# Kernel optimization log

Measured on AMD Instinct MI355X. Metric: run time of the kernel, lower is better.

The kernel has to match this reference:

```python
import jax, jax.numpy as jnp
import numpy as np

BITS = 8
BOUND = 2 ** (BITS - 1) - 1  # 127, symmetric int8 as in AQT IntNumerics


def setup_inputs() -> dict:
    key = jax.random.key(0)
    k1, k2 = jax.random.split(key)
    lhs = jax.random.normal(k1, (8192, 4096), dtype=jnp.float32)
    rhs = jax.random.normal(k2, (4096, 4096), dtype=jnp.float32)
    return {"lhs": lhs, "rhs": rhs}


def reference(lhs, rhs):
    # Per-channel symmetric scales over the contracting dim (AQT calibration:
    # abs-max / bound). lhs contracts axis 1, rhs contracts axis 0, per
    # dimension_numbers (((1,),(0,)),((),())).
    lhs_scale = jnp.max(jnp.abs(lhs), axis=1, keepdims=True) / BOUND  # [M,1]
    rhs_scale = jnp.max(jnp.abs(rhs), axis=0, keepdims=True) / BOUND  # [1,N]
    lhs_scale = jnp.where(lhs_scale == 0, jnp.ones_like(lhs_scale), lhs_scale)
    rhs_scale = jnp.where(rhs_scale == 0, jnp.ones_like(rhs_scale), rhs_scale)

    # Quantize: round-to-nearest, clip to [-127, 127], store as int8.
    qlhs = jnp.clip(jnp.round(lhs / lhs_scale), -BOUND, BOUND).astype(jnp.int8)
    qrhs = jnp.clip(jnp.round(rhs / rhs_scale), -BOUND, BOUND).astype(jnp.int8)

    # Integer matmul with int32 accumulation (the AQT quantized dot_general).
    acc = jax.lax.dot_general(
        qlhs, qrhs,
        dimension_numbers=(((1,), (0,)), ((), ())),
        preferred_element_type=jnp.int32,
    )  # [M, N] int32

    # Inline dequant by transposed scales (scale_t): [M,1] * [1,N].
    return acc.astype(jnp.float32) * lhs_scale * rhs_scale
```

## Files before the change

### kernel.cpp

```cpp
#include <hip/hip_runtime.h>
#include <stdint.h>

#define M_DIM 8192
#define N_DIM 4096
#define K_DIM 4096

typedef int v4i __attribute__((ext_vector_type(4)));

typedef __attribute__((address_space(1))) const void gas_void;
typedef __attribute__((address_space(3))) void las_void;

__device__ __forceinline__ void async_copy16(const uint8_t* g, uint8_t* l) {
    __builtin_amdgcn_global_load_lds((gas_void*)g, (las_void*)l, 16, 0, 0);
}

__device__ __forceinline__ int quant1(float x, float scale) {
    float q = __builtin_rintf(x / scale);
    q = fminf(127.0f, fmaxf(-127.0f, q));
    return (int)q;
}

__device__ __forceinline__ uint32_t pack4(int q0, int q1, int q2, int q3) {
    return (uint32_t)(q0 & 255) | ((uint32_t)(q1 & 255) << 8) |
           ((uint32_t)(q2 & 255) << 16) | ((uint32_t)(q3 & 255) << 24);
}

__global__ __launch_bounds__(256) void quant_lhs_kernel(
    const float* __restrict__ lhs, uint8_t* __restrict__ qlhs,
    float* __restrict__ lhs_scale) {
    const int row = blockIdx.x;
    const int tid = threadIdx.x;
    const float4* src = (const float4*)(lhs + (size_t)row * K_DIM);

    float4 v[4];
    float m = 0.0f;
#pragma unroll
    for (int i = 0; i < 4; ++i) {
        v[i] = src[tid + i * 256];
        m = fmaxf(m, fmaxf(fmaxf(fabsf(v[i].x), fabsf(v[i].y)),
                           fmaxf(fabsf(v[i].z), fabsf(v[i].w))));
    }
#pragma unroll
    for (int off = 32; off > 0; off >>= 1)
        m = fmaxf(m, __shfl_down(m, off, 64));

    __shared__ float wmax[4];
    if ((tid & 63) == 0) wmax[tid >> 6] = m;
    __syncthreads();
    const float mm = fmaxf(fmaxf(wmax[0], wmax[1]), fmaxf(wmax[2], wmax[3]));
    const float scale = (mm == 0.0f) ? 1.0f : mm / 127.0f;
    if (tid == 0) lhs_scale[row] = scale;

    uint32_t* dst = (uint32_t*)(qlhs + (size_t)row * K_DIM);
#pragma unroll
    for (int i = 0; i < 4; ++i) {
        dst[tid + i * 256] = pack4(quant1(v[i].x, scale), quant1(v[i].y, scale),
                                   quant1(v[i].z, scale), quant1(v[i].w, scale));
    }
}

__global__ __launch_bounds__(256) void rhs_max_kernel(
    const float* __restrict__ rhs, uint32_t* __restrict__ maxbits) {
    const int c = blockIdx.x * 256 + threadIdx.x;
    const int r0 = blockIdx.y * 32;
    float m = 0.0f;
#pragma unroll
    for (int r = 0; r < 32; ++r)
        m = fmaxf(m, fabsf(rhs[(size_t)(r0 + r) * N_DIM + c]));
    atomicMax(&maxbits[c], __float_as_uint(m));
}

__global__ __launch_bounds__(256) void quant_rhs_t_kernel(
    const float* __restrict__ rhs, const uint32_t* __restrict__ maxbits,
    uint8_t* __restrict__ qrhsT) {
    __shared__ __align__(16) uint8_t tile[64 * 132];
    const int nbase = blockIdx.x * 64;
    const int kbase = blockIdx.y * 128;
    const int tid = threadIdx.x;

    const int n0 = (tid & 15) * 4;
    float s[4];
#pragma unroll
    for (int j = 0; j < 4; ++j) {
        const float m = __uint_as_float(maxbits[nbase + n0 + j]);
        s[j] = (m == 0.0f) ? 1.0f : m / 127.0f;
    }

#pragma unroll
    for (int p = 0; p < 2; ++p) {
        const int k0 = (tid >> 4) * 4 + p * 64;
        int q[4][4];
#pragma unroll
        for (int i = 0; i < 4; ++i) {
            const float4 v = *(const float4*)(
                rhs + (size_t)(kbase + k0 + i) * N_DIM + nbase + n0);
            q[i][0] = quant1(v.x, s[0]);
            q[i][1] = quant1(v.y, s[1]);
            q[i][2] = quant1(v.z, s[2]);
            q[i][3] = quant1(v.w, s[3]);
        }
#pragma unroll
        for (int j = 0; j < 4; ++j) {
            *(uint32_t*)(tile + (n0 + j) * 132 + k0) =
                pack4(q[0][j], q[1][j], q[2][j], q[3][j]);
        }
    }
    __syncthreads();

#pragma unroll
    for (int p = 0; p < 2; ++p) {
        const int c = tid + p * 256;
        const int n = c >> 3;
        const int g = c & 7;
        uint32_t d[4];
#pragma unroll
        for (int w = 0; w < 4; ++w)
            d[w] = *(const uint32_t*)(tile + n * 132 + g * 16 + w * 4);
        uint4 u;
        u.x = d[0]; u.y = d[1]; u.z = d[2]; u.w = d[3];
        *(uint4*)(qrhsT + (size_t)(nbase + n) * K_DIM + kbase + g * 16) = u;
    }
}

__global__ __launch_bounds__(512, 2) void gemm_i8_kernel(
    const uint8_t* __restrict__ qlhs, const uint8_t* __restrict__ qrhsT,
    const float* __restrict__ lhs_scale, const uint32_t* __restrict__ maxbits,
    float* __restrict__ out) {
    extern __shared__ __align__(16) uint8_t smem[];

    const int tid = threadIdx.x;
    const int wave = tid >> 6;
    const int lane = tid & 63;

    const int bm = blockIdx.y * 256;
    const int bn = blockIdx.x * 256;

    const int srow = tid >> 2;
    const int gsrc = (((tid & 3) ^ ((tid >> 3) & 3)) << 4);
    const uint8_t* gA = qlhs + (size_t)(bm + srow) * K_DIM + gsrc;
    const uint8_t* gA2 = gA + (size_t)128 * K_DIM;
    const uint8_t* gB = qrhsT + (size_t)(bn + srow) * K_DIM + gsrc;
    const uint8_t* gB2 = gB + (size_t)128 * K_DIM;
    const uint32_t stO = (uint32_t)tid * 16u;

    const int wm = (wave >> 2) * 128;
    const int wn = (wave & 3) * 64;
    const uint32_t fg = (uint32_t)((((lane >> 4) ^ ((lane >> 1) & 3)) << 4));
    const uint32_t aoff = (uint32_t)((wm + (lane & 15)) * 64) + fg;
    const uint32_t boff = 16384u + (uint32_t)((wn + (lane & 15)) * 64) + fg;

    v4i acc[8][4] = {};

#define BARRIER() __builtin_amdgcn_s_barrier()
#define LGKM0()                                            \
    do {                                                   \
        asm volatile("s_waitcnt lgkmcnt(0)" ::: "memory"); \
        __builtin_amdgcn_sched_barrier(0);                 \
    } while (0)

#pragma unroll
    for (int p = 0; p < 3; ++p) {
        uint8_t* sb = smem + (p << 15);
        async_copy16(gA, sb + stO);
        async_copy16(gA2, sb + 8192 + stO);
        async_copy16(gB, sb + 16384 + stO);
        async_copy16(gB2, sb + 24576 + stO);
        gA += 64; gA2 += 64; gB += 64; gB2 += 64;
    }
    asm volatile("s_waitcnt vmcnt(8)" ::: "memory");
    BARRIER();

#pragma unroll 1
    for (int tt = 0; tt < 64; tt += 4) {
#pragma unroll
        for (int u = 0; u < 4; ++u) {
            const int t = tt + u;
            uint8_t* const Cb = smem + (u << 15);
            uint8_t* const Sb = smem + (((u + 3) & 3) << 15);

            v4i a[4], b[4];

#pragma unroll
            for (int i = 0; i < 4; ++i)
                a[i] = *(const v4i*)(Cb + aoff + i * 1024);
#pragma unroll
            for (int i = 0; i < 4; ++i)
                b[i] = *(const v4i*)(Cb + boff + i * 1024);
            async_copy16(gA, Sb + stO);
            async_copy16(gA2, Sb + 8192 + stO);
            BARRIER();
            LGKM0();
            __builtin_amdgcn_s_setprio(1);
#pragma unroll
            for (int mi = 0; mi < 4; ++mi)
#pragma unroll
                for (int ni = 0; ni < 4; ++ni)
                    acc[mi][ni] = __builtin_amdgcn_mfma_i32_16x16x64_i8(
                        a[mi], b[ni], acc[mi][ni], 0, 0, 0);
            __builtin_amdgcn_s_setprio(0);
            BARRIER();

#pragma unroll
            for (int i = 0; i < 4; ++i)
                a[i] = *(const v4i*)(Cb + aoff + (4 + i) * 1024);
            async_copy16(gB, Sb + 16384 + stO);
            async_copy16(gB2, Sb + 24576 + stO);
            if (t < 60) {
                gA += 64; gA2 += 64; gB += 64; gB2 += 64;
            }
            BARRIER();
            LGKM0();
            __builtin_amdgcn_s_setprio(1);
#pragma unroll
            for (int mi = 0; mi < 4; ++mi)
#pragma unroll
                for (int ni = 0; ni < 4; ++ni)
                    acc[4 + mi][ni] = __builtin_amdgcn_mfma_i32_16x16x64_i8(
                        a[mi], b[ni], acc[4 + mi][ni], 0, 0, 0);
            __builtin_amdgcn_s_setprio(0);
            asm volatile("s_waitcnt vmcnt(8)" ::: "memory");
            BARRIER();
        }
    }
    asm volatile("s_waitcnt vmcnt(0)" ::: "memory");

    const int r0 = bm + wm + (lane >> 4) * 4;
    const int c0 = bn + wn + (lane & 15);
    float rsv[4];
#pragma unroll
    for (int ni = 0; ni < 4; ++ni) {
        const float m = __uint_as_float(maxbits[c0 + ni * 16]);
        rsv[ni] = (m == 0.0f) ? 1.0f : m / 127.0f;
    }
#pragma unroll
    for (int mi = 0; mi < 8; ++mi) {
        float ls[4];
#pragma unroll
        for (int r = 0; r < 4; ++r) ls[r] = lhs_scale[r0 + mi * 16 + r];
#pragma unroll
        for (int ni = 0; ni < 4; ++ni) {
            float* o = out + (size_t)(r0 + mi * 16) * N_DIM + c0 + ni * 16;
#pragma unroll
            for (int r = 0; r < 4; ++r)
                o[(size_t)r * N_DIM] = (float)acc[mi][ni][r] * ls[r] * rsv[ni];
        }
    }
#undef BARRIER
#undef LGKM0
}

extern "C" void kernel_launch(void* const* d_in, const int* in_sizes, int n_in,
                              void* d_out, int out_size, void* d_ws,
                              size_t ws_size, hipStream_t stream) {
    const float* lhs = (const float*)d_in[0];
    const float* rhs = (const float*)d_in[1];
    float* out = (float*)d_out;

    uint8_t* ws = (uint8_t*)d_ws;
    uint8_t* qlhs = ws;
    uint8_t* qrhsT = ws + 33554432u;
    float* lhs_scale = (float*)(ws + 50331648u);
    uint32_t* maxbits = (uint32_t*)(ws + 50380800u);

    static bool attr_set = false;
    if (!attr_set) {
        hipFuncSetAttribute((const void*)gemm_i8_kernel,
                            hipFuncAttributeMaxDynamicSharedMemorySize,
                            131072);
        attr_set = true;
    }

    hipMemsetAsync(maxbits, 0, N_DIM * sizeof(uint32_t), stream);

    quant_lhs_kernel<<<M_DIM, 256, 0, stream>>>(lhs, qlhs, lhs_scale);
    rhs_max_kernel<<<dim3(N_DIM / 256, 128), 256, 0, stream>>>(rhs, maxbits);
    quant_rhs_t_kernel<<<dim3(N_DIM / 64, K_DIM / 128), 256, 0, stream>>>(
        rhs, maxbits, qrhsT);
    gemm_i8_kernel<<<dim3(N_DIM / 256, M_DIM / 256), 512, 131072, stream>>>(
        qlhs, qrhsT, lhs_scale, maxbits, out);
}
```

Before: 403.7 us.

## Interleave LDS loads with MFMAs, remap blocks per XCD, vectorize rhs max

```diff
diff --git a/kernel.cpp b/kernel.cpp
--- a/kernel.cpp
+++ b/kernel.cpp
@@ -61,13 +61,21 @@
 
 __global__ __launch_bounds__(256) void rhs_max_kernel(
     const float* __restrict__ rhs, uint32_t* __restrict__ maxbits) {
-    const int c = blockIdx.x * 256 + threadIdx.x;
+    const int c4 = (blockIdx.x * 256 + threadIdx.x) * 4;
     const int r0 = blockIdx.y * 32;
-    float m = 0.0f;
-#pragma unroll
-    for (int r = 0; r < 32; ++r)
-        m = fmaxf(m, fabsf(rhs[(size_t)(r0 + r) * N_DIM + c]));
-    atomicMax(&maxbits[c], __float_as_uint(m));
+    float m0 = 0.0f, m1 = 0.0f, m2 = 0.0f, m3 = 0.0f;
+#pragma unroll
+    for (int r = 0; r < 32; ++r) {
+        const float4 v = *(const float4*)(rhs + (size_t)(r0 + r) * N_DIM + c4);
+        m0 = fmaxf(m0, fabsf(v.x));
+        m1 = fmaxf(m1, fabsf(v.y));
+        m2 = fmaxf(m2, fabsf(v.z));
+        m3 = fmaxf(m3, fabsf(v.w));
+    }
+    atomicMax(&maxbits[c4 + 0], __float_as_uint(m0));
+    atomicMax(&maxbits[c4 + 1], __float_as_uint(m1));
+    atomicMax(&maxbits[c4 + 2], __float_as_uint(m2));
+    atomicMax(&maxbits[c4 + 3], __float_as_uint(m3));
 }
 
 __global__ __launch_bounds__(256) void quant_rhs_t_kernel(
@@ -132,8 +140,13 @@
     const int wave = tid >> 6;
     const int lane = tid & 63;
 
-    const int bm = blockIdx.y * 256;
-    const int bn = blockIdx.x * 256;
+    const int obid = blockIdx.y * 16 + blockIdx.x;
+    const int xcd = obid & 7;
+    const int local = obid >> 3;
+    const int ty = (xcd >> 1) * 8 + (local >> 3);
+    const int tx = (xcd & 1) * 8 + (local & 7);
+    const int bm = ty * 256;
+    const int bn = tx * 256;
 
     const int srow = tid >> 2;
     const int gsrc = (((tid & 3) ^ ((tid >> 3) & 3)) << 4);
@@ -151,11 +164,22 @@
 
     v4i acc[8][4] = {};
 
-#define BARRIER() __builtin_amdgcn_s_barrier()
-#define LGKM0()                                            \
-    do {                                                   \
-        asm volatile("s_waitcnt lgkmcnt(0)" ::: "memory"); \
-        __builtin_amdgcn_sched_barrier(0);                 \
+#define FENCE() asm volatile("" ::: "memory")
+#define LGKM(n)                                                 \
+    do {                                                        \
+        asm volatile("s_waitcnt lgkmcnt(" #n ")" ::: "memory"); \
+        __builtin_amdgcn_sched_barrier(0);                      \
+    } while (0)
+#define MFMA4(mi, av)                                                          \
+    do {                                                                       \
+        acc[mi][0] =                                                           \
+            __builtin_amdgcn_mfma_i32_16x16x64_i8(av, vb0, acc[mi][0], 0, 0, 0); \
+        acc[mi][1] =                                                           \
+            __builtin_amdgcn_mfma_i32_16x16x64_i8(av, vb1, acc[mi][1], 0, 0, 0); \
+        acc[mi][2] =                                                           \
+            __builtin_amdgcn_mfma_i32_16x16x64_i8(av, vb2, acc[mi][2], 0, 0, 0); \
+        acc[mi][3] =                                                           \
+            __builtin_amdgcn_mfma_i32_16x16x64_i8(av, vb3, acc[mi][3], 0, 0, 0); \
     } while (0)
 
 #pragma unroll
@@ -168,58 +192,56 @@
         gA += 64; gA2 += 64; gB += 64; gB2 += 64;
     }
     asm volatile("s_waitcnt vmcnt(8)" ::: "memory");
-    BARRIER();
+    __builtin_amdgcn_s_barrier();
 
 #pragma unroll 1
     for (int tt = 0; tt < 64; tt += 4) {
 #pragma unroll
         for (int u = 0; u < 4; ++u) {
             const int t = tt + u;
-            uint8_t* const Cb = smem + (u << 15);
+            const uint8_t* const Cb = smem + (u << 15);
             uint8_t* const Sb = smem + (((u + 3) & 3) << 15);
 
-            v4i a[4], b[4];
-
-#pragma unroll
-            for (int i = 0; i < 4; ++i)
-                a[i] = *(const v4i*)(Cb + aoff + i * 1024);
-#pragma unroll
-            for (int i = 0; i < 4; ++i)
-                b[i] = *(const v4i*)(Cb + boff + i * 1024);
+            v4i vb0, vb1, vb2, vb3;
+            v4i va0, va1, va2, va3, va4, va5, va6, va7;
+
+            vb0 = *(const v4i*)(Cb + boff + 0);
+            vb1 = *(const v4i*)(Cb + boff + 1024);
+            vb2 = *(const v4i*)(Cb + boff + 2048);
+            vb3 = *(const v4i*)(Cb + boff + 3072);
+            va0 = *(const v4i*)(Cb + aoff + 0);
+            FENCE();
+            va1 = *(const v4i*)(Cb + aoff + 1024);
+            FENCE();
+
             async_copy16(gA, Sb + stO);
             async_copy16(gA2, Sb + 8192 + stO);
-            BARRIER();
-            LGKM0();
-            __builtin_amdgcn_s_setprio(1);
-#pragma unroll
-            for (int mi = 0; mi < 4; ++mi)
-#pragma unroll
-                for (int ni = 0; ni < 4; ++ni)
-                    acc[mi][ni] = __builtin_amdgcn_mfma_i32_16x16x64_i8(
-                        a[mi], b[ni], acc[mi][ni], 0, 0, 0);
-            __builtin_amdgcn_s_setprio(0);
-            BARRIER();
-
-#pragma unroll
-            for (int i = 0; i < 4; ++i)
-                a[i] = *(const v4i*)(Cb + aoff + (4 + i) * 1024);
             async_copy16(gB, Sb + 16384 + stO);
             async_copy16(gB2, Sb + 24576 + stO);
             if (t < 60) {
                 gA += 64; gA2 += 64; gB += 64; gB2 += 64;
             }
-            BARRIER();
-            LGKM0();
+            FENCE();
+
             __builtin_amdgcn_s_setprio(1);
-#pragma unroll
-            for (int mi = 0; mi < 4; ++mi)
-#pragma unroll
-                for (int ni = 0; ni < 4; ++ni)
-                    acc[4 + mi][ni] = __builtin_amdgcn_mfma_i32_16x16x64_i8(
-                        a[mi], b[ni], acc[4 + mi][ni], 0, 0, 0);
+            LGKM(1);  MFMA4(0, va0);
+            va2 = *(const v4i*)(Cb + aoff + 2048); FENCE();
+            LGKM(1);  MFMA4(1, va1);
+            va3 = *(const v4i*)(Cb + aoff + 3072); FENCE();
+            LGKM(1);  MFMA4(2, va2);
+            va4 = *(const v4i*)(Cb + aoff + 4096); FENCE();
+            LGKM(1);  MFMA4(3, va3);
+            va5 = *(const v4i*)(Cb + aoff + 5120); FENCE();
+            LGKM(1);  MFMA4(4, va4);
+            va6 = *(const v4i*)(Cb + aoff + 6144); FENCE();
+            LGKM(1);  MFMA4(5, va5);
+            va7 = *(const v4i*)(Cb + aoff + 7168); FENCE();
+            LGKM(1);  MFMA4(6, va6);
+            LGKM(0);  MFMA4(7, va7);
             __builtin_amdgcn_s_setprio(0);
+
             asm volatile("s_waitcnt vmcnt(8)" ::: "memory");
-            BARRIER();
+            __builtin_amdgcn_s_barrier();
         }
     }
     asm volatile("s_waitcnt vmcnt(0)" ::: "memory");
@@ -245,8 +267,9 @@
                 o[(size_t)r * N_DIM] = (float)acc[mi][ni][r] * ls[r] * rsv[ni];
         }
     }
-#undef BARRIER
-#undef LGKM0
+#undef FENCE
+#undef LGKM
+#undef MFMA4
 }
 
 extern "C" void kernel_launch(void* const* d_in, const int* in_sizes, int n_in,
@@ -273,7 +296,7 @@
     hipMemsetAsync(maxbits, 0, N_DIM * sizeof(uint32_t), stream);
 
     quant_lhs_kernel<<<M_DIM, 256, 0, stream>>>(lhs, qlhs, lhs_scale);
-    rhs_max_kernel<<<dim3(N_DIM / 256, 128), 256, 0, stream>>>(rhs, maxbits);
+    rhs_max_kernel<<<dim3(N_DIM / 1024, 128), 256, 0, stream>>>(rhs, maxbits);
     quant_rhs_t_kernel<<<dim3(N_DIM / 64, K_DIM / 128), 256, 0, stream>>>(
         rhs, maxbits, qrhsT);
     gemm_i8_kernel<<<dim3(N_DIM / 256, M_DIM / 256), 512, 131072, stream>>>(
```

Result: no change. 408.9 us (+1.3%).
